# Optimization experiments

Measured on AMD Instinct MI355X. Metric: run time of the kernel, lower is better.

Reference implementation:

```python
import jax, jax.numpy as jnp
import numpy as np
import random as pyrandom

NUM_CENTERS = 512
NUM_ITERS = 10
EPS = 1e-16
SEED = 42


def setup_inputs() -> dict:
    key = jax.random.key(0)
    x = jax.random.normal(key, (4, 16384, 256), dtype=jnp.float32)
    return {"x": x}


def _get_dist(x, v):
    # squared Euclidean distances: [B, N, K]
    x2 = jnp.sum(x * x, axis=-1, keepdims=True)            # [B, N, 1]
    xv = jnp.einsum('bnd,bkd->bnk', x, v)                  # [B, N, K]
    v2 = jnp.sum(v * v, axis=-1)[:, None, :]               # [B, 1, K]
    return jax.nn.relu(x2 - 2.0 * xv + v2)


def _update_u(x, v):
    clusters = jnp.argmin(_get_dist(x, v), axis=-1)        # [B, N]
    return jax.nn.one_hot(clusters, NUM_CENTERS, dtype=x.dtype)  # [B, N, K]


def _update_v(x, u):
    # normalize memberships over the points axis (torch dim=1 == axis -2 here)
    un = (u + EPS) / (jnp.sum(u, axis=-2, keepdims=True) + EPS)
    return jnp.einsum('bnk,bnd->bkd', un, x)               # [B, K, d]


def reference(x):
    n = x.shape[-2]
    pyrandom.seed(SEED)
    inds = np.asarray(pyrandom.sample(range(n), NUM_CENTERS))
    # initialization happens under no_grad in the original module
    v0 = jax.lax.stop_gradient(x[..., inds, :])            # [B, K, d]
    u0 = jax.lax.stop_gradient(_update_u(x, v0))

    def step(carry, _):
        _, v = carry
        u_new = _update_u(x, v)
        v_new = _update_v(x, u_new)
        return (u_new, v_new), None

    (u, v), _ = jax.lax.scan(step, (u0, v0), None, length=NUM_ITERS)
    return (u, v)
```

## Files before the change

### kernel.cpp

```cpp
#include <hip/hip_runtime.h>
#include <string.h>

#define B 4
#define N 16384
#define D 256
#define K 512
#define ITERS 10

typedef short short8 __attribute__((ext_vector_type(8)));
typedef float float4v __attribute__((ext_vector_type(4)));

static void host_sample_inds(int* out) {
    static unsigned int mt[624];
    mt[0] = 19650218u;
    for (int i = 1; i < 624; i++)
        mt[i] = 1812433253u * (mt[i - 1] ^ (mt[i - 1] >> 30)) + (unsigned)i;
    {
        int i = 1, j = 0;
        for (int kk = 624; kk; kk--) {
            mt[i] = (mt[i] ^ ((mt[i - 1] ^ (mt[i - 1] >> 30)) * 1664525u)) + 42u + (unsigned)j;
            i++; j++;
            if (i >= 624) { mt[0] = mt[623]; i = 1; }
            if (j >= 1) j = 0;
        }
        for (int kk = 623; kk; kk--) {
            mt[i] = (mt[i] ^ ((mt[i - 1] ^ (mt[i - 1] >> 30)) * 1566083941u)) - (unsigned)i;
            i++;
            if (i >= 624) { mt[0] = mt[623]; i = 1; }
        }
        mt[0] = 0x80000000u;
    }
    static unsigned char seen[N];
    memset(seen, 0, sizeof(seen));
    int mti = 624;
    int got = 0;
    while (got < K) {
        if (mti >= 624) {
            for (int kk = 0; kk < 624; kk++) {
                unsigned int yy = (mt[kk] & 0x80000000u) | (mt[(kk + 1) % 624] & 0x7fffffffu);
                mt[kk] = mt[(kk + 397) % 624] ^ (yy >> 1) ^ ((yy & 1u) ? 0x9908b0dfu : 0u);
            }
            mti = 0;
        }
        unsigned int y = mt[mti++];
        y ^= y >> 11; y ^= (y << 7) & 0x9d2c5680u; y ^= (y << 15) & 0xefc60000u; y ^= y >> 18;
        unsigned int r = y >> 17;
        if (r >= (unsigned)N) continue;
        if (seen[r]) continue;
        seen[r] = 1;
        out[got++] = (int)r;
    }
}

__device__ inline void gload_lds16(const void* g, void* l) {
    __builtin_amdgcn_global_load_lds((const __attribute__((address_space(1))) void*)g,
                                     (__attribute__((address_space(3))) void*)l, 16, 0, 0);
}

__device__ inline unsigned bf16_rne(float f) {
    unsigned u = __float_as_uint(f);
    return (u + 0x7fffu + ((u >> 16) & 1u)) >> 16;
}

__device__ inline unsigned long long shfl_xor_u64(unsigned long long v, int off) {
    int lo = __shfl_xor((int)(unsigned)(v & 0xffffffffull), off);
    int hi = __shfl_xor((int)(unsigned)(v >> 32), off);
    return ((unsigned long long)(unsigned)hi << 32) | (unsigned)lo;
}


__global__ void k_gather_v0(const float* __restrict__ x, const int* __restrict__ inds,
                            float* __restrict__ v) {
    int bk = blockIdx.x; int b = bk / K, k = bk % K;
    int n = inds[k];
    const float4* src = (const float4*)(x + ((size_t)b * N + n) * D);
    float4* dst = (float4*)(v + ((size_t)b * K + k) * D);
    dst[threadIdx.x] = src[threadIdx.x];
}

__global__ void k_totsum(const float* __restrict__ x, float* __restrict__ totsum) {
    int b = blockIdx.y;
    int n0 = blockIdx.x * (N / 64);
    int t = threadIdx.x;
    const float* xb = x + (size_t)b * N * D;
    float s = 0.f;
    int n = n0;
    for (; n + 4 <= n0 + N / 64; n += 4) {
        float a0 = xb[(size_t)n * D + t];
        float a1 = xb[(size_t)(n + 1) * D + t];
        float a2 = xb[(size_t)(n + 2) * D + t];
        float a3 = xb[(size_t)(n + 3) * D + t];
        s += a0; s += a1; s += a2; s += a3;
    }
    for (; n < n0 + N / 64; n++) s += xb[(size_t)n * D + t];
    atomicAdd(&totsum[b * D + t], s);
}

__global__ void k_prep(const float* __restrict__ src, unsigned short* __restrict__ cat,
                       float* __restrict__ sq, float* __restrict__ resn,
                       float* __restrict__ lon) {
    int wave = threadIdx.x >> 6, lane = threadIdx.x & 63;
    int row = blockIdx.x * 4 + wave;
    float4 f = ((const float4*)(src + (size_t)row * D))[lane];
    float comp[4] = {f.x, f.y, f.z, f.w};
    unsigned short h[4], l[4];
    float r2 = 0.f, l2 = 0.f, n2 = 0.f;
    #pragma unroll
    for (int j = 0; j < 4; j++) {
        n2 += comp[j] * comp[j];
        unsigned hi = bf16_rne(comp[j]);
        float hif = __uint_as_float(hi << 16);
        float r = comp[j] - hif;
        unsigned lo = bf16_rne(r);
        float lof = __uint_as_float(lo << 16);
        float res = r - lof;
        r2 += res * res;
        l2 += lof * lof;
        h[j] = (unsigned short)hi; l[j] = (unsigned short)lo;
    }
    unsigned short* orow = cat + (size_t)row * 512;
    *(ushort4*)&orow[lane * 4] = make_ushort4(h[0], h[1], h[2], h[3]);
    *(ushort4*)&orow[256 + lane * 4] = make_ushort4(l[0], l[1], l[2], l[3]);
    #pragma unroll
    for (int off = 32; off; off >>= 1) {
        r2 += __shfl_xor(r2, off);
        l2 += __shfl_xor(l2, off);
        n2 += __shfl_xor(n2, off);
    }
    if (lane == 0) { sq[row] = n2; resn[row] = sqrtf(r2); lon[row] = sqrtf(l2); }
}

__global__ void k_errmax(const float* __restrict__ v2, const float* __restrict__ vres,
                         const float* __restrict__ vlo,
                         float* __restrict__ vmaxs, float* __restrict__ vresmaxs,
                         float* __restrict__ vlomaxs) {
    __shared__ float s1[256], s2[256], s3[256];
    int b = blockIdx.x, t = threadIdx.x;
    s1[t] = fmaxf(sqrtf(v2[b * K + t]), sqrtf(v2[b * K + 256 + t]));
    s2[t] = fmaxf(vres[b * K + t], vres[b * K + 256 + t]);
    s3[t] = fmaxf(vlo[b * K + t], vlo[b * K + 256 + t]);
    __syncthreads();
    for (int s = 128; s; s >>= 1) {
        if (t < s) {
            s1[t] = fmaxf(s1[t], s1[t + s]);
            s2[t] = fmaxf(s2[t], s2[t + s]);
            s3[t] = fmaxf(s3[t], s3[t + s]);
        }
        __syncthreads();
    }
    if (t == 0) { vmaxs[b] = s1[0]; vresmaxs[b] = s2[0]; vlomaxs[b] = s3[0]; }
}

__global__ void k_transpose(const float* __restrict__ v, float* __restrict__ vT) {
    int idx = blockIdx.x * 256 + threadIdx.x;
    int d = idx & 255, c = (idx >> 8) & 511, b = idx >> 17;
    vT[((size_t)b * D + d) * K + c] = v[idx];
}

__global__ __launch_bounds__(256, 2) void k_gemm_assign(
    const unsigned short* __restrict__ xcat, const unsigned short* __restrict__ vcat,
    const float* __restrict__ x2, const float* __restrict__ v2,
    const float* __restrict__ xres, const float* __restrict__ xlo,
    const float* __restrict__ vmaxs, const float* __restrict__ vresmaxs,
    const float* __restrict__ vlomaxs,
    int* __restrict__ assign, int* __restrict__ counts,
    int* __restrict__ refine_cnt, int* __restrict__ refine_pt) {
    __shared__ __align__(16) unsigned short As[2][128 * 64];
    __shared__ __align__(16) unsigned short Bs[2][128 * 64];
    __shared__ float x2s[128];
    __shared__ float v2s[512];
    __shared__ unsigned long long candk[128][2][2];
    int b = blockIdx.y;
    int n0 = blockIdx.x * 128;
    int tid = threadIdx.x;
    int wv = tid >> 6, lane = tid & 63;
    int wr = wv >> 1, wc = wv & 1;
    int quad = lane >> 4, l16 = lane & 15;
    const unsigned short* xb = xcat + ((size_t)b * N + n0) * 512;
    const unsigned short* vb0 = vcat + (size_t)b * K * 512;

    if (tid < 128) x2s[tid] = x2[b * N + n0 + tid];
    v2s[tid] = v2[b * K + tid];
    v2s[tid + 256] = v2[b * K + 256 + tid];

    int lds8[4], srow[4], schunk[4];
    #pragma unroll
    for (int i = 0; i < 4; i++) {
        int l = i * 256 + wv * 64 + lane;
        lds8[i] = l * 8;
        srow[i] = l >> 3;
        schunk[i] = ((l & 7) ^ ((l >> 3) & 7)) * 8;
    }

    float4v acc[4][4];
    #pragma unroll
    for (int i = 0; i < 4; i++)
        #pragma unroll
        for (int j = 0; j < 4; j++) acc[i][j] = (float4v){0.f, 0.f, 0.f, 0.f};

    unsigned long long k1[16], k2[16];
    #pragma unroll
    for (int i = 0; i < 16; i++) { k1[i] = ~0ull; k2[i] = ~0ull; }

    #pragma unroll
    for (int i = 0; i < 4; i++) {
        gload_lds16(xb + (size_t)srow[i] * 512 + schunk[i], (void*)&As[0][lds8[i]]);
        gload_lds16(vb0 + (size_t)srow[i] * 512 + schunk[i], (void*)&Bs[0][lds8[i]]);
    }
    __syncthreads();

    for (int ch = 0; ch < 4; ch++) {
        for (int kt = 0; kt < 12; kt++) {
            int cur = kt & 1;
            int nkt = kt + 1, nch = ch;
            if (nkt == 12) { nkt = 0; nch++; }
            if (nch < 4) {
                int k4 = (nkt & 3) * 64;
                int kcolA = (nkt < 8) ? k4 : 256 + k4;
                int kcolB = (nkt < 4) ? k4 : ((nkt < 8) ? 256 + k4 : k4);
                const unsigned short* vbn = vb0 + (size_t)nch * (128 * 512);
                #pragma unroll
                for (int i = 0; i < 4; i++) {
                    gload_lds16(xb + (size_t)srow[i] * 512 + kcolA + schunk[i],
                                (void*)&As[1 - cur][lds8[i]]);
                    gload_lds16(vbn + (size_t)srow[i] * 512 + kcolB + schunk[i],
                                (void*)&Bs[1 - cur][lds8[i]]);
                }
            }
            #pragma unroll
            for (int ks = 0; ks < 2; ks++) {
                short8 af[4], bf[4];
                int ccr = ks * 4 + quad;
                #pragma unroll
                for (int f = 0; f < 4; f++) {
                    int rA = wr * 64 + f * 16 + l16;
                    af[f] = *(const short8*)&As[cur][(rA * 8 + (ccr ^ (rA & 7))) * 8];
                    int rB = wc * 64 + f * 16 + l16;
                    bf[f] = *(const short8*)&Bs[cur][(rB * 8 + (ccr ^ (rB & 7))) * 8];
                }
                #pragma unroll
                for (int fi = 0; fi < 4; fi++)
                    #pragma unroll
                    for (int fj = 0; fj < 4; fj++)
                        acc[fi][fj] = __builtin_amdgcn_mfma_f32_16x16x32_bf16(
                            af[fi], bf[fj], acc[fi][fj], 0, 0, 0);
            }
            __syncthreads();
        }
        #pragma unroll
        for (int fi = 0; fi < 4; fi++) {
            #pragma unroll
            for (int r = 0; r < 4; r++) {
                int lrow = wr * 64 + fi * 16 + quad * 4 + r;
                float x2v = x2s[lrow];
                int idx = fi * 4 + r;
                #pragma unroll
                for (int fj = 0; fj < 4; fj++) {
                    int cg = ch * 128 + wc * 64 + fj * 16 + l16;
                    float dist = fmaxf((x2v - 2.0f * acc[fi][fj][r]) + v2s[cg], 0.0f);
                    unsigned long long key =
                        ((unsigned long long)__float_as_uint(dist) << 32) | (unsigned)cg;
                    if (key < k1[idx]) { k2[idx] = k1[idx]; k1[idx] = key; }
                    else if (key < k2[idx]) { k2[idx] = key; }
                }
            }
        }
        #pragma unroll
        for (int fi = 0; fi < 4; fi++)
            #pragma unroll
            for (int fj = 0; fj < 4; fj++) acc[fi][fj] = (float4v){0.f, 0.f, 0.f, 0.f};
    }

    #pragma unroll
    for (int fi = 0; fi < 4; fi++) {
        #pragma unroll
        for (int r = 0; r < 4; r++) {
            int lrow = wr * 64 + fi * 16 + quad * 4 + r;
            int idx = fi * 4 + r;
            unsigned long long a1 = k1[idx], a2 = k2[idx];
            #pragma unroll
            for (int off = 1; off < 16; off <<= 1) {
                unsigned long long o1 = shfl_xor_u64(a1, off);
                unsigned long long o2 = shfl_xor_u64(a2, off);
                unsigned long long mx = a1 > o1 ? a1 : o1;
                a1 = a1 < o1 ? a1 : o1;
                unsigned long long mn2 = a2 < o2 ? a2 : o2;
                a2 = mx < mn2 ? mx : mn2;
            }
            if (l16 == 0) { candk[lrow][wc][0] = a1; candk[lrow][wc][1] = a2; }
        }
    }
    __syncthreads();
    if (tid < 128) {
        unsigned long long a1 = candk[tid][0][0], a2 = candk[tid][0][1];
        unsigned long long o1 = candk[tid][1][0], o2 = candk[tid][1][1];
        unsigned long long mx = a1 > o1 ? a1 : o1;
        unsigned long long b1 = a1 < o1 ? a1 : o1;
        unsigned long long mn2 = a2 < o2 ? a2 : o2;
        unsigned long long b2 = mx < mn2 ? mx : mn2;
        float bv1 = __uint_as_float((unsigned)(b1 >> 32));
        float bv2 = __uint_as_float((unsigned)(b2 >> 32));
        int bi1 = (int)(unsigned)(b1 & 0xffffffffull);
        int p = b * N + n0 + tid;
        assign[p] = bi1;
        atomicAdd(&counts[b * K + bi1], 1);
        float thr = 4.0f * (xres[p] * vmaxs[b] + sqrtf(x2s[tid]) * vresmaxs[b]
                            + xlo[p] * vlomaxs[b]) + 4e-3f;
        if (bv2 - bv1 < thr) {
            int pos = atomicAdd(refine_cnt, 1);
            refine_pt[pos] = p;
        }
    }
}

__global__ __launch_bounds__(256) void k_rescan(
    const float* __restrict__ x, const float* __restrict__ vT,
    const float* __restrict__ x2, const float* __restrict__ v2,
    const int* __restrict__ refine_cnt, const int* __restrict__ refine_pt,
    int* __restrict__ assign, int* __restrict__ counts) {
    __shared__ float xs[256];
    __shared__ float rv[256];
    __shared__ int ri[256];
    int cnt = *refine_cnt;
    int t = threadIdx.x;
    for (int i = blockIdx.x; i < cnt; i += gridDim.x) {
        int p = refine_pt[i];
        int b = p >> 14;
        xs[t] = x[(size_t)p * D + t];
        __syncthreads();
        const float* vtb = vT + (size_t)b * D * K;
        float s0 = 0.f, s1 = 0.f;
        for (int d = 0; d < D; d++) {
            float xd = xs[d];
            s0 = fmaf(xd, vtb[(size_t)d * K + t], s0);
            s1 = fmaf(xd, vtb[(size_t)d * K + 256 + t], s1);
        }
        float x2p = x2[p];
        float d0 = fmaxf((x2p - 2.0f * s0) + v2[b * K + t], 0.0f);
        float d1 = fmaxf((x2p - 2.0f * s1) + v2[b * K + 256 + t], 0.0f);
        float bv; int bi;
        if (d1 < d0) { bv = d1; bi = t + 256; } else { bv = d0; bi = t; }
        rv[t] = bv; ri[t] = bi;
        __syncthreads();
        for (int s = 128; s; s >>= 1) {
            if (t < s) {
                if (rv[t + s] < rv[t] || (rv[t + s] == rv[t] && ri[t + s] < ri[t])) {
                    rv[t] = rv[t + s]; ri[t] = ri[t + s];
                }
            }
            __syncthreads();
        }
        if (t == 0) {
            int old = assign[p];
            int neu = ri[0];
            if (neu != old) {
                assign[p] = neu;
                atomicSub(&counts[b * K + old], 1);
                atomicAdd(&counts[b * K + neu], 1);
            }
        }
        __syncthreads();
    }
}


__global__ __launch_bounds__(256) void k_scatter(
    const int* __restrict__ assign, const int* __restrict__ counts,
    int* __restrict__ cursor, int* __restrict__ order) {
    __shared__ int offs[K];
    int b = blockIdx.y;
    if (threadIdx.x < 64) {
        int lane = threadIdx.x;
        int pre[8]; int s = 0;
        #pragma unroll
        for (int j = 0; j < 8; j++) { pre[j] = s; s += counts[b * K + lane * 8 + j]; }
        int inc = s;
        #pragma unroll
        for (int off = 1; off < 64; off <<= 1) {
            int o = __shfl_up(inc, off);
            if (lane >= off) inc += o;
        }
        int excl = inc - s;
        #pragma unroll
        for (int j = 0; j < 8; j++) offs[lane * 8 + j] = excl + pre[j];
    }
    __syncthreads();
    int n = blockIdx.x * 256 + threadIdx.x;
    int a = assign[b * N + n];
    int pos = atomicAdd(&cursor[b * K + a], 1);
    order[b * N + offs[a] + pos] = n;
}

__global__ __launch_bounds__(256) void k_sumdiv(
    const float* __restrict__ x, const int* __restrict__ counts,
    const int* __restrict__ order, const float* __restrict__ totsum,
    float* __restrict__ v) {
    __shared__ int sh[256];
    __shared__ int ord[256];
    int t = threadIdx.x;
    int b = blockIdx.y, k = blockIdx.x;
    const int* cb = counts + b * K;
    int partial = 0;
    for (int j = t; j < k; j += 256) partial += cb[j];
    sh[t] = partial; __syncthreads();
    for (int s = 128; s; s >>= 1) { if (t < s) sh[t] += sh[t + s]; __syncthreads(); }
    int off = sh[0];
    int cnt = cb[k];
    const float* xb = x + (size_t)b * N * D;
    float acc = 0.f;
    for (int m0 = 0; m0 < cnt; m0 += 256) {
        int mm = min(256, cnt - m0);
        if (t < mm) ord[t] = order[b * N + off + m0 + t];
        __syncthreads();
        int m = 0;
        for (; m + 4 <= mm; m += 4) {
            int i0 = ord[m], i1 = ord[m + 1], i2 = ord[m + 2], i3 = ord[m + 3];
            float a0 = xb[(size_t)i0 * D + t];
            float a1 = xb[(size_t)i1 * D + t];
            float a2 = xb[(size_t)i2 * D + t];
            float a3 = xb[(size_t)i3 * D + t];
            acc += a0; acc += a1; acc += a2; acc += a3;
        }
        for (; m < mm; m++) {
            int n = ord[m];
            acc += xb[(size_t)n * D + t];
        }
        __syncthreads();
    }
    float out;
    if (cnt > 0) out = acc * (1.0f / (float)cnt);
    else out = totsum[b * D + t];
    v[((size_t)b * K + k) * D + t] = out;
}

__global__ void k_write_u(const int* __restrict__ assign, float* __restrict__ uout) {
    int idx = blockIdx.x * 256 + threadIdx.x;
    int a = assign[idx];
    uout[(size_t)idx * K + a] = 1.0f;
}

__global__ void k_copy_v(const float* __restrict__ v, float* __restrict__ out) {
    int idx = blockIdx.x * 256 + threadIdx.x;
    ((float4*)out)[idx] = ((const float4*)v)[idx];
}

extern "C" void kernel_launch(void* const* d_in, const int* in_sizes, int n_in,
                              void* d_out, int out_size, void* d_ws, size_t ws_size,
                              hipStream_t stream) {
    const float* x = (const float*)d_in[0];
    float* out = (float*)d_out;
    char* ws = (char*)d_ws;

    size_t off = 0;
    float* v      = (float*)(ws + off); off += (size_t)B * K * D * 4;
    float* x2     = (float*)(ws + off); off += (size_t)B * N * 4;
    float* v2     = (float*)(ws + off); off += (size_t)B * K * 4;
    float* totsum = (float*)(ws + off); off += (size_t)B * D * 4;
    int* assign   = (int*)(ws + off);   off += (size_t)B * N * 4;
    int* counts   = (int*)(ws + off);   off += (size_t)B * K * 4;
    int* cursor   = (int*)(ws + off);   off += (size_t)B * K * 4;
    int* order    = (int*)(ws + off);   off += (size_t)B * N * 4;
    int* inds     = (int*)(ws + off);   off += 4096;
    int* refine_cnt = (int*)(ws + off); off += 256;

    char* ob = (char*)out;
    size_t oboff = 0;
    unsigned short* xcat = (unsigned short*)(ob + oboff); oboff += (size_t)B * N * 512 * 2;
    int* refine_pt = (int*)(ob + oboff);    oboff += (size_t)B * N * 4;
    float* vT      = (float*)(ob + oboff);  oboff += (size_t)B * K * D * 4;
    float* xres    = (float*)(ob + oboff);  oboff += (size_t)B * N * 4;
    float* xlo     = (float*)(ob + oboff);  oboff += (size_t)B * N * 4;
    float* vres    = (float*)(ob + oboff);  oboff += (size_t)B * K * 4;
    float* vlo     = (float*)(ob + oboff);  oboff += (size_t)B * K * 4;
    float* vmaxs   = (float*)(ob + oboff);  oboff += 256;
    float* vresmaxs = (float*)(ob + oboff); oboff += 256;
    float* vlomaxs = (float*)(ob + oboff);  oboff += 256;
    unsigned short* vcat = (unsigned short*)(out + (size_t)B * N * K);

    static int h_inds[K];
    host_sample_inds(h_inds);
    hipMemcpyAsync(inds, h_inds, K * sizeof(int), hipMemcpyHostToDevice, stream);

    hipMemsetAsync(totsum, 0, (size_t)B * D * 4, stream);
    k_gather_v0<<<B * K, 64, 0, stream>>>(x, inds, v);
    k_totsum<<<dim3(64, B), 256, 0, stream>>>(x, totsum);
    k_prep<<<(B * N) / 4, 256, 0, stream>>>(x, xcat, x2, xres, xlo);

    for (int it = 0; it < ITERS; it++) {
        k_prep<<<(B * K) / 4, 256, 0, stream>>>(v, vcat, v2, vres, vlo);
        k_errmax<<<B, 256, 0, stream>>>(v2, vres, vlo, vmaxs, vresmaxs, vlomaxs);
        k_transpose<<<(B * K * D) / 256, 256, 0, stream>>>(v, vT);
        hipMemsetAsync(refine_cnt, 0, 256, stream);
        hipMemsetAsync(counts, 0, 2 * (size_t)B * K * 4, stream);
        k_gemm_assign<<<dim3(N / 128, B), 256, 0, stream>>>(
            xcat, vcat, x2, v2, xres, xlo, vmaxs, vresmaxs, vlomaxs,
            assign, counts, refine_cnt, refine_pt);
        k_rescan<<<1024, 256, 0, stream>>>(x, vT, x2, v2, refine_cnt, refine_pt,
                                           assign, counts);
        k_scatter<<<dim3(N / 256, B), 256, 0, stream>>>(assign, counts, cursor, order);
        k_sumdiv<<<dim3(K, B), 256, 0, stream>>>(x, counts, order, totsum, v);
    }

    hipMemsetAsync(out, 0, (size_t)B * N * K * 4, stream);
    k_write_u<<<(B * N) / 256, 256, 0, stream>>>(assign, out);
    k_copy_v<<<(B * K * D) / 1024, 256, 0, stream>>>(v, out + (size_t)B * N * K);
}
```

Before: 1.710 ms.

## Fuse errmax and transpose into prep/sumdiv, batch rescan points per block

Drops the separate k_errmax and k_transpose launches. The per-batch max reductions now happen inside k_prep through float atomicMax, and vT is written directly by k_gather_v0 and k_sumdiv. The memsets are merged into one, and the refine list is split per batch. k_rescan now handles 8 points per block so each vT load is reused across all 8. This cuts launch overhead and redundant passes over vT, at the cost of strided vT writes in sumdiv and extra register pressure in rescan.

```diff
diff --git a/kernel.cpp b/kernel.cpp
--- a/kernel.cpp
+++ b/kernel.cpp
@@ -70,12 +70,18 @@
 
 
 __global__ void k_gather_v0(const float* __restrict__ x, const int* __restrict__ inds,
-                            float* __restrict__ v) {
+                            float* __restrict__ v, float* __restrict__ vT) {
     int bk = blockIdx.x; int b = bk / K, k = bk % K;
     int n = inds[k];
+    int t = threadIdx.x;
     const float4* src = (const float4*)(x + ((size_t)b * N + n) * D);
     float4* dst = (float4*)(v + ((size_t)b * K + k) * D);
-    dst[threadIdx.x] = src[threadIdx.x];
+    float4 f = src[t];
+    dst[t] = f;
+    float comp[4] = {f.x, f.y, f.z, f.w};
+    #pragma unroll
+    for (int j = 0; j < 4; j++)
+        vT[((size_t)b * D + t * 4 + j) * K + k] = comp[j];
 }
 
 __global__ void k_totsum(const float* __restrict__ x, float* __restrict__ totsum) {
@@ -98,7 +104,8 @@
 
 __global__ void k_prep(const float* __restrict__ src, unsigned short* __restrict__ cat,
                        float* __restrict__ sq, float* __restrict__ resn,
-                       float* __restrict__ lon) {
+                       float* __restrict__ lon, float* maxbuf) {
+    __shared__ float red[3][4];
     int wave = threadIdx.x >> 6, lane = threadIdx.x & 63;
     int row = blockIdx.x * 4 + wave;
     float4 f = ((const float4*)(src + (size_t)row * D))[lane];
@@ -127,42 +134,30 @@
         l2 += __shfl_xor(l2, off);
         n2 += __shfl_xor(n2, off);
     }
-    if (lane == 0) { sq[row] = n2; resn[row] = sqrtf(r2); lon[row] = sqrtf(l2); }
-}
-
-__global__ void k_errmax(const float* __restrict__ v2, const float* __restrict__ vres,
-                         const float* __restrict__ vlo,
-                         float* __restrict__ vmaxs, float* __restrict__ vresmaxs,
-                         float* __restrict__ vlomaxs) {
-    __shared__ float s1[256], s2[256], s3[256];
-    int b = blockIdx.x, t = threadIdx.x;
-    s1[t] = fmaxf(sqrtf(v2[b * K + t]), sqrtf(v2[b * K + 256 + t]));
-    s2[t] = fmaxf(vres[b * K + t], vres[b * K + 256 + t]);
-    s3[t] = fmaxf(vlo[b * K + t], vlo[b * K + 256 + t]);
-    __syncthreads();
-    for (int s = 128; s; s >>= 1) {
-        if (t < s) {
-            s1[t] = fmaxf(s1[t], s1[t + s]);
-            s2[t] = fmaxf(s2[t], s2[t + s]);
-            s3[t] = fmaxf(s3[t], s3[t + s]);
-        }
+    float rn = sqrtf(r2), ln = sqrtf(l2);
+    if (lane == 0) {
+        sq[row] = n2; resn[row] = rn; lon[row] = ln;
+        if (maxbuf) { red[0][wave] = n2; red[1][wave] = rn; red[2][wave] = ln; }
+    }
+    if (maxbuf) {
         __syncthreads();
-    }
-    if (t == 0) { vmaxs[b] = s1[0]; vresmaxs[b] = s2[0]; vlomaxs[b] = s3[0]; }
-}
-
-__global__ void k_transpose(const float* __restrict__ v, float* __restrict__ vT) {
-    int idx = blockIdx.x * 256 + threadIdx.x;
-    int d = idx & 255, c = (idx >> 8) & 511, b = idx >> 17;
-    vT[((size_t)b * D + d) * K + c] = v[idx];
+        if (threadIdx.x == 0) {
+            int b = row >> 9;
+            float m0 = fmaxf(fmaxf(red[0][0], red[0][1]), fmaxf(red[0][2], red[0][3]));
+            float m1 = fmaxf(fmaxf(red[1][0], red[1][1]), fmaxf(red[1][2], red[1][3]));
+            float m2 = fmaxf(fmaxf(red[2][0], red[2][1]), fmaxf(red[2][2], red[2][3]));
+            atomicMax((unsigned int*)&maxbuf[b], __float_as_uint(m0));
+            atomicMax((unsigned int*)&maxbuf[16 + b], __float_as_uint(m1));
+            atomicMax((unsigned int*)&maxbuf[32 + b], __float_as_uint(m2));
+        }
+    }
 }
 
 __global__ __launch_bounds__(256, 2) void k_gemm_assign(
     const unsigned short* __restrict__ xcat, const unsigned short* __restrict__ vcat,
     const float* __restrict__ x2, const float* __restrict__ v2,
     const float* __restrict__ xres, const float* __restrict__ xlo,
-    const float* __restrict__ vmaxs, const float* __restrict__ vresmaxs,
-    const float* __restrict__ vlomaxs,
+    const float* __restrict__ maxbuf,
     int* __restrict__ assign, int* __restrict__ counts,
     int* __restrict__ refine_cnt, int* __restrict__ refine_pt) {
     __shared__ __align__(16) unsigned short As[2][128 * 64];
@@ -304,62 +299,81 @@
         int p = b * N + n0 + tid;
         assign[p] = bi1;
         atomicAdd(&counts[b * K + bi1], 1);
-        float thr = 4.0f * (xres[p] * vmaxs[b] + sqrtf(x2s[tid]) * vresmaxs[b]
-                            + xlo[p] * vlomaxs[b]) + 4e-3f;
+        float thr = 4.0f * (xres[p] * sqrtf(maxbuf[b]) + sqrtf(x2s[tid]) * maxbuf[16 + b]
+                            + xlo[p] * maxbuf[32 + b]) + 4e-3f;
         if (bv2 - bv1 < thr) {
-            int pos = atomicAdd(refine_cnt, 1);
-            refine_pt[pos] = p;
-        }
-    }
-}
-
+            int pos = atomicAdd(&refine_cnt[b], 1);
+            refine_pt[b * N + pos] = p;
+        }
+    }
+}
+
+#define RPTS 8
 __global__ __launch_bounds__(256) void k_rescan(
     const float* __restrict__ x, const float* __restrict__ vT,
     const float* __restrict__ x2, const float* __restrict__ v2,
     const int* __restrict__ refine_cnt, const int* __restrict__ refine_pt,
     int* __restrict__ assign, int* __restrict__ counts) {
-    __shared__ float xs[256];
+    __shared__ float xs[RPTS][256];
+    __shared__ int pj[RPTS];
     __shared__ float rv[256];
     __shared__ int ri[256];
-    int cnt = *refine_cnt;
     int t = threadIdx.x;
-    for (int i = blockIdx.x; i < cnt; i += gridDim.x) {
-        int p = refine_pt[i];
-        int b = p >> 14;
-        xs[t] = x[(size_t)p * D + t];
-        __syncthreads();
-        const float* vtb = vT + (size_t)b * D * K;
-        float s0 = 0.f, s1 = 0.f;
-        for (int d = 0; d < D; d++) {
-            float xd = xs[d];
-            s0 = fmaf(xd, vtb[(size_t)d * K + t], s0);
-            s1 = fmaf(xd, vtb[(size_t)d * K + 256 + t], s1);
-        }
-        float x2p = x2[p];
-        float d0 = fmaxf((x2p - 2.0f * s0) + v2[b * K + t], 0.0f);
-        float d1 = fmaxf((x2p - 2.0f * s1) + v2[b * K + 256 + t], 0.0f);
-        float bv; int bi;
-        if (d1 < d0) { bv = d1; bi = t + 256; } else { bv = d0; bi = t; }
-        rv[t] = bv; ri[t] = bi;
-        __syncthreads();
-        for (int s = 128; s; s >>= 1) {
-            if (t < s) {
-                if (rv[t + s] < rv[t] || (rv[t + s] == rv[t] && ri[t + s] < ri[t])) {
-                    rv[t] = rv[t + s]; ri[t] = ri[t + s];
+    for (int bb = 0; bb < B; bb++) {
+        int cnt = refine_cnt[bb];
+        int ngroups = (cnt + RPTS - 1) / RPTS;
+        const float* vtb = vT + (size_t)bb * D * K;
+        for (int g = blockIdx.x; g < ngroups; g += gridDim.x) {
+            int base = g * RPTS;
+            int np = min(RPTS, cnt - base);
+            for (int j = 0; j < np; j++) {
+                int p = refine_pt[bb * N + base + j];
+                if (t == 0) pj[j] = p;
+                xs[j][t] = x[(size_t)p * D + t];
+            }
+            __syncthreads();
+            float s0[RPTS], s1[RPTS];
+            #pragma unroll
+            for (int j = 0; j < RPTS; j++) { s0[j] = 0.f; s1[j] = 0.f; }
+            for (int d = 0; d < D; d++) {
+                float vt0 = vtb[(size_t)d * K + t];
+                float vt1 = vtb[(size_t)d * K + 256 + t];
+                #pragma unroll
+                for (int j = 0; j < RPTS; j++) {
+                    s0[j] = fmaf(xs[j][d], vt0, s0[j]);
+                    s1[j] = fmaf(xs[j][d], vt1, s1[j]);
                 }
             }
-            __syncthreads();
-        }
-        if (t == 0) {
-            int old = assign[p];
-            int neu = ri[0];
-            if (neu != old) {
-                assign[p] = neu;
-                atomicSub(&counts[b * K + old], 1);
-                atomicAdd(&counts[b * K + neu], 1);
-            }
-        }
-        __syncthreads();
+            float v20 = v2[bb * K + t], v21 = v2[bb * K + 256 + t];
+            for (int j = 0; j < np; j++) {
+                int p = pj[j];
+                float x2p = x2[p];
+                float d0 = fmaxf((x2p - 2.0f * s0[j]) + v20, 0.0f);
+                float d1 = fmaxf((x2p - 2.0f * s1[j]) + v21, 0.0f);
+                float bv; int bi;
+                if (d1 < d0) { bv = d1; bi = t + 256; } else { bv = d0; bi = t; }
+                rv[t] = bv; ri[t] = bi;
+                __syncthreads();
+                for (int s = 128; s; s >>= 1) {
+                    if (t < s) {
+                        if (rv[t + s] < rv[t] || (rv[t + s] == rv[t] && ri[t + s] < ri[t])) {
+                            rv[t] = rv[t + s]; ri[t] = ri[t + s];
+                        }
+                    }
+                    __syncthreads();
+                }
+                if (t == 0) {
+                    int old = assign[p];
+                    int neu = ri[0];
+                    if (neu != old) {
+                        assign[p] = neu;
+                        atomicSub(&counts[bb * K + old], 1);
+                        atomicAdd(&counts[bb * K + neu], 1);
+                    }
+                }
+                __syncthreads();
+            }
+        }
     }
 }
 
@@ -394,7 +408,7 @@
 __global__ __launch_bounds__(256) void k_sumdiv(
     const float* __restrict__ x, const int* __restrict__ counts,
     const int* __restrict__ order, const float* __restrict__ totsum,
-    float* __restrict__ v) {
+    float* __restrict__ v, float* __restrict__ vT) {
     __shared__ int sh[256];
     __shared__ int ord[256];
     int t = threadIdx.x;
@@ -431,6 +445,7 @@
     if (cnt > 0) out = acc * (1.0f / (float)cnt);
     else out = totsum[b * D + t];
     v[((size_t)b * K + k) * D + t] = out;
+    vT[((size_t)b * D + t) * K + k] = out;
 }
 
 __global__ void k_write_u(const int* __restrict__ assign, float* __restrict__ uout) {
@@ -457,11 +472,13 @@
     float* v2     = (float*)(ws + off); off += (size_t)B * K * 4;
     float* totsum = (float*)(ws + off); off += (size_t)B * D * 4;
     int* assign   = (int*)(ws + off);   off += (size_t)B * N * 4;
+    int* order    = (int*)(ws + off);   off += (size_t)B * N * 4;
+    int* inds     = (int*)(ws + off);   off += 4096;
     int* counts   = (int*)(ws + off);   off += (size_t)B * K * 4;
     int* cursor   = (int*)(ws + off);   off += (size_t)B * K * 4;
-    int* order    = (int*)(ws + off);   off += (size_t)B * N * 4;
-    int* inds     = (int*)(ws + off);   off += 4096;
     int* refine_cnt = (int*)(ws + off); off += 256;
+    float* maxbuf = (float*)(ws + off); off += 256;
+    size_t zero_bytes = 2 * (size_t)B * K * 4 + 512;
 
     char* ob = (char*)out;
     size_t oboff = 0;
@@ -472,9 +489,6 @@
     float* xlo     = (float*)(ob + oboff);  oboff += (size_t)B * N * 4;
     float* vres    = (float*)(ob + oboff);  oboff += (size_t)B * K * 4;
     float* vlo     = (float*)(ob + oboff);  oboff += (size_t)B * K * 4;
-    float* vmaxs   = (float*)(ob + oboff);  oboff += 256;
-    float* vresmaxs = (float*)(ob + oboff); oboff += 256;
-    float* vlomaxs = (float*)(ob + oboff);  oboff += 256;
     unsigned short* vcat = (unsigned short*)(out + (size_t)B * N * K);
 
     static int h_inds[K];
@@ -482,23 +496,20 @@
     hipMemcpyAsync(inds, h_inds, K * sizeof(int), hipMemcpyHostToDevice, stream);
 
     hipMemsetAsync(totsum, 0, (size_t)B * D * 4, stream);
-    k_gather_v0<<<B * K, 64, 0, stream>>>(x, inds, v);
+    k_gather_v0<<<B * K, 64, 0, stream>>>(x, inds, v, vT);
     k_totsum<<<dim3(64, B), 256, 0, stream>>>(x, totsum);
-    k_prep<<<(B * N) / 4, 256, 0, stream>>>(x, xcat, x2, xres, xlo);
+    k_prep<<<(B * N) / 4, 256, 0, stream>>>(x, xcat, x2, xres, xlo, nullptr);
 
     for (int it = 0; it < ITERS; it++) {
-        k_prep<<<(B * K) / 4, 256, 0, stream>>>(v, vcat, v2, vres, vlo);
-        k_errmax<<<B, 256, 0, stream>>>(v2, vres, vlo, vmaxs, vresmaxs, vlomaxs);
-        k_transpose<<<(B * K * D) / 256, 256, 0, stream>>>(v, vT);
-        hipMemsetAsync(refine_cnt, 0, 256, stream);
-        hipMemsetAsync(counts, 0, 2 * (size_t)B * K * 4, stream);
+        hipMemsetAsync(counts, 0, zero_bytes, stream);
+        k_prep<<<(B * K) / 4, 256, 0, stream>>>(v, vcat, v2, vres, vlo, maxbuf);
         k_gemm_assign<<<dim3(N / 128, B), 256, 0, stream>>>(
-            xcat, vcat, x2, v2, xres, xlo, vmaxs, vresmaxs, vlomaxs,
+            xcat, vcat, x2, v2, xres, xlo, maxbuf,
             assign, counts, refine_cnt, refine_pt);
         k_rescan<<<1024, 256, 0, stream>>>(x, vT, x2, v2, refine_cnt, refine_pt,
                                            assign, counts);
         k_scatter<<<dim3(N / 256, B), 256, 0, stream>>>(assign, counts, cursor, order);
-        k_sumdiv<<<dim3(K, B), 256, 0, stream>>>(x, counts, order, totsum, v);
+        k_sumdiv<<<dim3(K, B), 256, 0, stream>>>(x, counts, order, totsum, v, vT);
     }
 
     hipMemsetAsync(out, 0, (size_t)B * N * K * 4, stream);
```

After: 2.882 ms. 68.5% more time.
